# Performance work log

Measured on AMD Instinct MI355X. Metric: run time of the kernel, lower is better.

The kernel has to match this reference:

```python
import jax, jax.numpy as jnp
import numpy as np

B, T, H, W, D = 8, 16, 64, 64, 256
DK = 128
TOP_K = 4
DECAY = 0.95
TAU = 1.0
EPS = 1e-10


def setup_inputs() -> dict:
    key = jax.random.key(0)
    ks = jax.random.split(key, 6)
    return {
        "query_features": jax.random.normal(ks[0], (B, H, W, D), dtype=jnp.float32),
        "history_buffer": jax.random.normal(ks[1], (B, T, H, W, D), dtype=jnp.float32),
        "W_q": jax.random.normal(ks[2], (D, DK), dtype=jnp.float32) * (1.0 / np.sqrt(D)),
        "W_k": jax.random.normal(ks[3], (D, DK), dtype=jnp.float32) * (1.0 / np.sqrt(D)),
        "W_v": jax.random.normal(ks[4], (D, DK), dtype=jnp.float32) * (1.0 / np.sqrt(D)),
        "W_o": jax.random.normal(ks[5], (DK, D), dtype=jnp.float32) * (1.0 / np.sqrt(DK)),
    }


def reference(query_features, history_buffer, W_q, W_k, W_v, W_o):
    # Projections (Linear, bias=False)
    Q = jnp.einsum("bhwd,dk->bhwk", query_features, W_q)          # [B,H,W,DK]
    K = jnp.einsum("bthwd,dk->bthwk", history_buffer, W_k)        # [B,T,H,W,DK]
    V = jnp.einsum("bthwd,dk->bthwk", history_buffer, W_v)        # [B,T,H,W,DK]

    # Per-pixel temporal scores over T history steps
    scores = jnp.einsum("bhwk,bthwk->bhwt", Q, K) / jnp.sqrt(jnp.float32(DK))  # [B,H,W,T]

    # Top-K gating over the time axis (top_k < T)
    _, topk_idx = jax.lax.top_k(scores, TOP_K)                    # [B,H,W,K]
    mask = jax.nn.one_hot(topk_idx, T, dtype=scores.dtype).sum(axis=-2) > 0  # [B,H,W,T]
    scores = jnp.where(mask, scores, -jnp.inf)

    # Log-decay bias: decay_rate ** (T - t)
    t = jnp.arange(T, dtype=jnp.float32)
    decay_bias = jnp.log(jnp.float32(DECAY) ** (T - t) + EPS)     # [T]
    scores = scores + decay_bias

    attn = jax.nn.softmax(scores / TAU, axis=-1)                  # [B,H,W,T]

    out = jnp.einsum("bhwt,bthwk->bhwk", attn, V)                 # [B,H,W,DK]
    out = jnp.einsum("bhwk,kd->bhwd", out, W_o)                   # [B,H,W,D]
    return out
```

## Files before the change

kernel.cpp:

```cpp
#include <hip/hip_runtime.h>
#include <math.h>


typedef __attribute__((ext_vector_type(8))) short bf16x8;
typedef __attribute__((ext_vector_type(4))) float f32x4;

__device__ inline unsigned short f2bf(float f) {
  union { float f; unsigned u; } v; v.f = f;
  unsigned r = (v.u + 0x7FFF + ((v.u >> 16) & 1)) >> 16;
  return (unsigned short)r;
}

__global__ __launch_bounds__(256) void precompute_weights(
    const float* __restrict__ Wq, const float* __restrict__ Wk,
    const float* __restrict__ Wv, const float* __restrict__ Wo,
    float* __restrict__ M1, unsigned short* __restrict__ M2F) {
  __shared__ float rowbuf[128];
  int bid = blockIdx.x, tid = threadIdx.x;
  if (bid < 256) {
    if (tid < 128) rowbuf[tid] = Wq[bid * 128 + tid];
    __syncthreads();
    const float4* Wk4 = (const float4*)Wk;
    const float4* rb4 = (const float4*)rowbuf;
    float acc = 0.f;
#pragma unroll 8
    for (int k4 = 0; k4 < 32; ++k4) {
      float4 a = rb4[k4];
      float4 b = Wk4[tid * 32 + k4];
      acc = fmaf(a.x, b.x, acc); acc = fmaf(a.y, b.y, acc);
      acc = fmaf(a.z, b.z, acc); acc = fmaf(a.w, b.w, acc);
    }
    M1[bid * 256 + tid] = acc;
  } else {
    int k = bid - 256;
    if (tid < 128) rowbuf[tid] = Wv[k * 128 + tid];
    __syncthreads();
    float acc = 0.f;
#pragma unroll 8
    for (int kk = 0; kk < 128; ++kk)
      acc = fmaf(rowbuf[kk], Wo[kk * 256 + tid], acc);
    int c = tid;
    int ct = c >> 4, kt = k >> 5, lh = (k >> 3) & 3, i = k & 7, lm = c & 15;
    M2F[(size_t)(((ct * 8 + kt) * 64 + lh * 16 + lm) * 8 + i)] = f2bf(acc);
  }
}

__global__ __launch_bounds__(256, 2) void fused_all(
    const float* __restrict__ query, const float* __restrict__ hist,
    const float* __restrict__ M1, const unsigned short* __restrict__ M2F,
    float* __restrict__ OUT) {
  __shared__ float As[64][260];
  int tid = threadIdx.x;
  int l = tid & 63;
  int w = tid >> 6;
  int pix0 = blockIdx.x * 64;

  const float4* H4 = (const float4*)hist;
  int b = pix0 >> 12;
  int off0 = pix0 & 4095;
  size_t hblk = ((size_t)b * 16 * 4096 + off0) * 64 + l;
  int t_mine = l & 15;
  int gbase = l & 48;

  {
    const float4* Qb4 = (const float4*)(query + (size_t)pix0 * 256);
#pragma unroll
    for (int k = 0; k < 16; ++k)
      *(float4*)&As[w + 4 * k][4 * l] = Qb4[(size_t)(w + 4 * k) * 64 + l];
    float4 acc[16];
#pragma unroll
    for (int j = 0; j < 16; ++j) acc[j] = make_float4(0.f, 0.f, 0.f, 0.f);
    const float4* B4 = (const float4*)M1;
#pragma unroll 4
    for (int d = 0; d < 256; ++d) {
      float4 bv = B4[d * 64 + l];
#pragma unroll
      for (int j = 0; j < 16; ++j) {
        float a = As[w + 4 * j][d];
        acc[j].x = fmaf(a, bv.x, acc[j].x);
        acc[j].y = fmaf(a, bv.y, acc[j].y);
        acc[j].z = fmaf(a, bv.z, acc[j].z);
        acc[j].w = fmaf(a, bv.w, acc[j].w);
      }
    }
#pragma unroll
    for (int j = 0; j < 16; ++j)
      *(float4*)&As[w + 4 * j][4 * l] = acc[j];
  }

  float4 hA[16], hB[16];
#pragma unroll
  for (int t = 0; t < 16; ++t)
    hA[t] = H4[hblk + (size_t)w * 64 + (size_t)t * 262144];

#define ATTN_STEP(HC, HN, IT, DOPRE)                                        \
  {                                                                         \
    int row = w + 4 * (IT);                                                 \
    if (DOPRE) {                   \
      size_t nb = hblk + (size_t)(row + 4) * 64;                            \
      _Pragma("unroll") for (int t = 0; t < 16; ++t)                        \
          HN[t] = H4[nb + (size_t)t * 262144];                              \
    }                                                                       \
    float4 q = *(const float4*)&As[row][4 * l];                             \
    float part[16];                                                         \
    _Pragma("unroll") for (int t = 0; t < 16; ++t) {                        \
      float s = HC[t].x * q.x;                                              \
      s = fmaf(HC[t].y, q.y, s);                                            \
      s = fmaf(HC[t].z, q.z, s);                                            \
      s = fmaf(HC[t].w, q.w, s);                                            \
      part[t] = s;                                                          \
    }                                                                       \
    _Pragma("unroll") for (int st = 0; st < 4; ++st) {                      \
      bool hi = (l >> st) & 1;                                              \
      int nt = 8 >> st;                                                     \
      _Pragma("unroll") for (int i = 0; i < nt; ++i) {                      \
        float mine = hi ? part[2 * i + 1] : part[2 * i];                    \
        float oth = hi ? part[2 * i] : part[2 * i + 1];                     \
        part[i] = mine + __shfl_xor(oth, 1 << st);                          \
      }                                                                     \
    }                                                                       \
    float v = part[0];                                                      \
    v += __shfl_xor(v, 16);                                                 \
    v += __shfl_xor(v, 32);                                                 \
    float sc = v * 0.08838834764831845f;         \
    int rank = 0;              \
    _Pragma("unroll") for (int k = 1; k < 16; ++k) {                        \
      int ot = (t_mine + k) & 15;                                           \
      float o = __shfl(sc, gbase | ot);                                     \
      rank += (o > sc) || (o == sc && ot < t_mine);                         \
    }                                                                       \
    bool chosen = rank < 4;                                                 \
    float earg = sc + (float)(16 - t_mine) * -0.05129329438755058f;         \
    float ex = chosen ? expf(earg) : 0.0f;                                  \
    float Z = ex;                                                           \
    Z += __shfl_xor(Z, 1);                                                  \
    Z += __shfl_xor(Z, 2);                                                  \
    Z += __shfl_xor(Z, 4);                                                  \
    Z += __shfl_xor(Z, 8);                                                  \
    float attn = ex / Z;                                                    \
    float4 hb = make_float4(0.f, 0.f, 0.f, 0.f);                            \
    _Pragma("unroll") for (int t = 0; t < 16; ++t) {                        \
      float a = __shfl(attn, gbase | t);  \
      if (a != 0.0f) {                                                      \
        hb.x = fmaf(a, HC[t].x, hb.x);                                      \
        hb.y = fmaf(a, HC[t].y, hb.y);                                      \
        hb.z = fmaf(a, HC[t].z, hb.z);                                      \
        hb.w = fmaf(a, HC[t].w, hb.w);                                      \
      }                                                                     \
    }                                                                       \
    *(float4*)&As[row][4 * l] = hb;   \
  }

  for (int it2 = 0; it2 < 8; ++it2) {
    ATTN_STEP(hA, hB, 2 * it2, true);
    ATTN_STEP(hB, hA, 2 * it2 + 1, it2 < 7);
  }
#undef ATTN_STEP

  {
    int lm = l & 15, lh = l >> 4;
    const bf16x8* B8 = (const bf16x8*)M2F;
    f32x4 acc[16];
#pragma unroll
    for (int ct = 0; ct < 16; ++ct) acc[ct] = (f32x4){0.f, 0.f, 0.f, 0.f};
#pragma unroll
    for (int kt = 0; kt < 8; ++kt) {
      const float* ap = &As[w + 4 * lm][kt * 32 + lh * 8];
      float4 a0 = *(const float4*)ap;
      float4 a1 = *(const float4*)(ap + 4);
      bf16x8 afrag;
      afrag[0] = (short)f2bf(a0.x); afrag[1] = (short)f2bf(a0.y);
      afrag[2] = (short)f2bf(a0.z); afrag[3] = (short)f2bf(a0.w);
      afrag[4] = (short)f2bf(a1.x); afrag[5] = (short)f2bf(a1.y);
      afrag[6] = (short)f2bf(a1.z); afrag[7] = (short)f2bf(a1.w);
#pragma unroll
      for (int ct = 0; ct < 16; ++ct) {
        bf16x8 bfrag = B8[(ct * 8 + kt) * 64 + l];
        acc[ct] = __builtin_amdgcn_mfma_f32_16x16x32_bf16(afrag, bfrag,
                                                          acc[ct], 0, 0, 0);
      }
    }
    float* outp = OUT + (size_t)pix0 * 256;
#pragma unroll
    for (int ct = 0; ct < 16; ++ct) {
#pragma unroll
      for (int j = 0; j < 4; ++j)
        outp[(size_t)(w + 4 * (lh * 4 + j)) * 256 + ct * 16 + lm] =
            acc[ct][j];
    }
  }
}

extern "C" void kernel_launch(void* const* d_in, const int* in_sizes, int n_in,
                              void* d_out, int out_size, void* d_ws,
                              size_t ws_size, hipStream_t stream) {
  const float* query = (const float*)d_in[0];
  const float* hist = (const float*)d_in[1];
  const float* Wq = (const float*)d_in[2];
  const float* Wk = (const float*)d_in[3];
  const float* Wv = (const float*)d_in[4];
  const float* Wo = (const float*)d_in[5];
  float* out = (float*)d_out;

  float* ws = (float*)d_ws;
  float* M1 = ws;
  unsigned short* M2F = (unsigned short*)(ws + 65536);

  precompute_weights<<<512, 256, 0, stream>>>(Wq, Wk, Wv, Wo, M1, M2F);
  fused_all<<<512, 256, 0, stream>>>(query, hist, M1, M2F, out);
}
```

Baseline: 170.7 us.

## Stream history per time step with running top-4 selection per pixel

New measurement: 185.5 us. 8.7% more time.

```diff
diff --git a/kernel.cpp b/kernel.cpp
--- a/kernel.cpp
+++ b/kernel.cpp
@@ -54,19 +54,22 @@
   int l = tid & 63;
   int w = tid >> 6;
   int pix0 = blockIdx.x * 64;
+  int r0 = w * 16;
 
   const float4* H4 = (const float4*)hist;
   int b = pix0 >> 12;
   int off0 = pix0 & 4095;
-  size_t hblk = ((size_t)b * 16 * 4096 + off0) * 64 + l;
-  int t_mine = l & 15;
-  int gbase = l & 48;
+  size_t habase = ((size_t)b * 65536 + off0 + r0) * 64 + l;
+
+  float4 hA[4], hB[4];
+#pragma unroll
+  for (int j = 0; j < 4; ++j) hA[j] = H4[habase + (size_t)j * 64];
 
   {
     const float4* Qb4 = (const float4*)(query + (size_t)pix0 * 256);
 #pragma unroll
     for (int k = 0; k < 16; ++k)
-      *(float4*)&As[w + 4 * k][4 * l] = Qb4[(size_t)(w + 4 * k) * 64 + l];
+      *(float4*)&As[r0 + k][4 * l] = Qb4[(size_t)(r0 + k) * 64 + l];
     float4 acc[16];
 #pragma unroll
     for (int j = 0; j < 16; ++j) acc[j] = make_float4(0.f, 0.f, 0.f, 0.f);
@@ -76,7 +79,7 @@
       float4 bv = B4[d * 64 + l];
 #pragma unroll
       for (int j = 0; j < 16; ++j) {
-        float a = As[w + 4 * j][d];
+        float a = As[r0 + j][d];
         acc[j].x = fmaf(a, bv.x, acc[j].x);
         acc[j].y = fmaf(a, bv.y, acc[j].y);
         acc[j].z = fmaf(a, bv.z, acc[j].z);
@@ -85,77 +88,108 @@
     }
 #pragma unroll
     for (int j = 0; j < 16; ++j)
-      *(float4*)&As[w + 4 * j][4 * l] = acc[j];
-  }
-
-  float4 hA[16], hB[16];
-#pragma unroll
-  for (int t = 0; t < 16; ++t)
-    hA[t] = H4[hblk + (size_t)w * 64 + (size_t)t * 262144];
-
-#define ATTN_STEP(HC, HN, IT, DOPRE)                                        \
+      *(float4*)&As[r0 + j][4 * l] = acc[j];
+  }
+
+#define STEP(HC, HN, T, PRE, NG4, NT)                                       \
   {                                                                         \
-    int row = w + 4 * (IT);                                                 \
-    if (DOPRE) {                   \
-      size_t nb = hblk + (size_t)(row + 4) * 64;                            \
-      _Pragma("unroll") for (int t = 0; t < 16; ++t)                        \
-          HN[t] = H4[nb + (size_t)t * 262144];                              \
-    }                                                                       \
-    float4 q = *(const float4*)&As[row][4 * l];                             \
-    float part[16];                                                         \
-    _Pragma("unroll") for (int t = 0; t < 16; ++t) {                        \
-      float s = HC[t].x * q.x;                                              \
-      s = fmaf(HC[t].y, q.y, s);                                            \
-      s = fmaf(HC[t].z, q.z, s);                                            \
-      s = fmaf(HC[t].w, q.w, s);                                            \
-      part[t] = s;                                                          \
-    }                                                                       \
-    _Pragma("unroll") for (int st = 0; st < 4; ++st) {                      \
-      bool hi = (l >> st) & 1;                                              \
-      int nt = 8 >> st;                                                     \
-      _Pragma("unroll") for (int i = 0; i < nt; ++i) {                      \
-        float mine = hi ? part[2 * i + 1] : part[2 * i];                    \
-        float oth = hi ? part[2 * i] : part[2 * i + 1];                     \
-        part[i] = mine + __shfl_xor(oth, 1 << st);                          \
+    if (PRE) {                                                              \
+      _Pragma("unroll") for (int j = 0; j < 4; ++j)                         \
+          HN[j] = H4[habase + (size_t)((NG4) + j) * 64 +                    \
+                     (size_t)(NT)*262144];                                  \
+    }                                                                       \
+    float pp[4];                                                            \
+    _Pragma("unroll") for (int j = 0; j < 4; ++j) {                         \
+      float s = HC[j].x * q[j].x;                                           \
+      s = fmaf(HC[j].y, q[j].y, s);                                         \
+      s = fmaf(HC[j].z, q[j].z, s);                                         \
+      s = fmaf(HC[j].w, q[j].w, s);                                         \
+      pp[j] = s;                                                            \
+    }                                                                       \
+    float sc[4];                                                            \
+    {                                                                       \
+      bool h1 = l & 1;                                                      \
+      float m0 = h1 ? pp[1] : pp[0], o0 = h1 ? pp[0] : pp[1];               \
+      float r0v = m0 + __shfl_xor(o0, 1);                                   \
+      float m1 = h1 ? pp[3] : pp[2], o1 = h1 ? pp[2] : pp[3];               \
+      float r1v = m1 + __shfl_xor(o1, 1);                                   \
+      bool h2 = l & 2;                                                      \
+      float m2 = h2 ? r1v : r0v, o2 = h2 ? r0v : r1v;                       \
+      float rr = m2 + __shfl_xor(o2, 2);                                    \
+      rr += __shfl_xor(rr, 4);                                              \
+      rr += __shfl_xor(rr, 8);                                              \
+      rr += __shfl_xor(rr, 16);                                             \
+      rr += __shfl_xor(rr, 32);                                             \
+      rr *= 0.08838834764831845f;                          \
+      _Pragma("unroll") for (int j = 0; j < 4; ++j)                         \
+          sc[j] = __shfl(rr, (l & 60) | j);                                 \
+    }                                                                       \
+    _Pragma("unroll") for (int j = 0; j < 4; ++j) {                         \
+      if ((T) < 4) {                                        \
+        ss[j][(T)] = sc[j]; stf[j][(T)] = (float)(T); sh[j][(T)] = HC[j];   \
+      } else {       \
+        float ms = ss[j][0], mt = stf[j][0]; int m = 0;                     \
+        _Pragma("unroll") for (int k = 1; k < 4; ++k) {                     \
+          bool wse = (ss[j][k] < ms) || (ss[j][k] == ms && stf[j][k] > mt); \
+          if (wse) { m = k; ms = ss[j][k]; mt = stf[j][k]; }                \
+        }                                                                   \
+        if (sc[j] > ms) {                          \
+          _Pragma("unroll") for (int k = 0; k < 4; ++k)                     \
+              if (m == k) {                                                 \
+            ss[j][k] = sc[j]; stf[j][k] = (float)(T); sh[j][k] = HC[j];     \
+          }                                                                 \
+        }                                                                   \
       }                                                                     \
     }                                                                       \
-    float v = part[0];                                                      \
-    v += __shfl_xor(v, 16);                                                 \
-    v += __shfl_xor(v, 32);                                                 \
-    float sc = v * 0.08838834764831845f;         \
-    int rank = 0;              \
-    _Pragma("unroll") for (int k = 1; k < 16; ++k) {                        \
-      int ot = (t_mine + k) & 15;                                           \
-      float o = __shfl(sc, gbase | ot);                                     \
-      rank += (o > sc) || (o == sc && ot < t_mine);                         \
-    }                                                                       \
-    bool chosen = rank < 4;                                                 \
-    float earg = sc + (float)(16 - t_mine) * -0.05129329438755058f;         \
-    float ex = chosen ? expf(earg) : 0.0f;                                  \
-    float Z = ex;                                                           \
-    Z += __shfl_xor(Z, 1);                                                  \
-    Z += __shfl_xor(Z, 2);                                                  \
-    Z += __shfl_xor(Z, 4);                                                  \
-    Z += __shfl_xor(Z, 8);                                                  \
-    float attn = ex / Z;                                                    \
-    float4 hb = make_float4(0.f, 0.f, 0.f, 0.f);                            \
-    _Pragma("unroll") for (int t = 0; t < 16; ++t) {                        \
-      float a = __shfl(attn, gbase | t);  \
-      if (a != 0.0f) {                                                      \
-        hb.x = fmaf(a, HC[t].x, hb.x);                                      \
-        hb.y = fmaf(a, HC[t].y, hb.y);                                      \
-        hb.z = fmaf(a, HC[t].z, hb.z);                                      \
-        hb.w = fmaf(a, HC[t].w, hb.w);                                      \
-      }                                                                     \
-    }                                                                       \
-    *(float4*)&As[row][4 * l] = hb;   \
-  }
-
-  for (int it2 = 0; it2 < 8; ++it2) {
-    ATTN_STEP(hA, hB, 2 * it2, true);
-    ATTN_STEP(hB, hA, 2 * it2 + 1, it2 < 7);
-  }
-#undef ATTN_STEP
+  }
+
+  for (int g = 0; g < 4; ++g) {
+    int g4 = g * 4;
+    float4 q[4];
+#pragma unroll
+    for (int j = 0; j < 4; ++j)
+      q[j] = *(const float4*)&As[r0 + g4 + j][4 * l];
+    float ss[4][4], stf[4][4];
+    float4 sh[4][4];
+
+    STEP(hA, hB, 0, 1, g4, 1)
+    STEP(hB, hA, 1, 1, g4, 2)
+    STEP(hA, hB, 2, 1, g4, 3)
+    STEP(hB, hA, 3, 1, g4, 4)
+    STEP(hA, hB, 4, 1, g4, 5)
+    STEP(hB, hA, 5, 1, g4, 6)
+    STEP(hA, hB, 6, 1, g4, 7)
+    STEP(hB, hA, 7, 1, g4, 8)
+    STEP(hA, hB, 8, 1, g4, 9)
+    STEP(hB, hA, 9, 1, g4, 10)
+    STEP(hA, hB, 10, 1, g4, 11)
+    STEP(hB, hA, 11, 1, g4, 12)
+    STEP(hA, hB, 12, 1, g4, 13)
+    STEP(hB, hA, 13, 1, g4, 14)
+    STEP(hA, hB, 14, 1, g4, 15)
+    STEP(hB, hA, 15, (g < 3), g4 + 4, 0)
+
+#pragma unroll
+    for (int j = 0; j < 4; ++j) {
+      float e0 = expf(ss[j][0] + (16.f - stf[j][0]) * -0.05129329438755058f);
+      float e1 = expf(ss[j][1] + (16.f - stf[j][1]) * -0.05129329438755058f);
+      float e2 = expf(ss[j][2] + (16.f - stf[j][2]) * -0.05129329438755058f);
+      float e3 = expf(ss[j][3] + (16.f - stf[j][3]) * -0.05129329438755058f);
+      float iZ = 1.0f / (e0 + e1 + e2 + e3);
+      float a0 = e0 * iZ, a1 = e1 * iZ, a2 = e2 * iZ, a3 = e3 * iZ;
+      float4 hb;
+      hb.x = a0 * sh[j][0].x; hb.y = a0 * sh[j][0].y;
+      hb.z = a0 * sh[j][0].z; hb.w = a0 * sh[j][0].w;
+      hb.x = fmaf(a1, sh[j][1].x, hb.x); hb.y = fmaf(a1, sh[j][1].y, hb.y);
+      hb.z = fmaf(a1, sh[j][1].z, hb.z); hb.w = fmaf(a1, sh[j][1].w, hb.w);
+      hb.x = fmaf(a2, sh[j][2].x, hb.x); hb.y = fmaf(a2, sh[j][2].y, hb.y);
+      hb.z = fmaf(a2, sh[j][2].z, hb.z); hb.w = fmaf(a2, sh[j][2].w, hb.w);
+      hb.x = fmaf(a3, sh[j][3].x, hb.x); hb.y = fmaf(a3, sh[j][3].y, hb.y);
+      hb.z = fmaf(a3, sh[j][3].z, hb.z); hb.w = fmaf(a3, sh[j][3].w, hb.w);
+      *(float4*)&As[r0 + g4 + j][4 * l] = hb;
+    }
+  }
+#undef STEP
 
   {
     int lm = l & 15, lh = l >> 4;
@@ -165,7 +199,7 @@
     for (int ct = 0; ct < 16; ++ct) acc[ct] = (f32x4){0.f, 0.f, 0.f, 0.f};
 #pragma unroll
     for (int kt = 0; kt < 8; ++kt) {
-      const float* ap = &As[w + 4 * lm][kt * 32 + lh * 8];
+      const float* ap = &As[r0 + lm][kt * 32 + lh * 8];
       float4 a0 = *(const float4*)ap;
       float4 a1 = *(const float4*)(ap + 4);
       bf16x8 afrag;
@@ -185,8 +219,7 @@
     for (int ct = 0; ct < 16; ++ct) {
 #pragma unroll
       for (int j = 0; j < 4; ++j)
-        outp[(size_t)(w + 4 * (lh * 4 + j)) * 256 + ct * 16 + lm] =
-            acc[ct][j];
+        outp[(size_t)(r0 + lh * 4 + j) * 256 + ct * 16 + lm] = acc[ct][j];
     }
   }
 }
```

## Split attention into score pass and sparse top-k gather of history rows

Applied to the files above, without the earlier changes.

Result: slower. 197.8 us (+15.9%).

```diff
diff --git a/kernel.cpp b/kernel.cpp
--- a/kernel.cpp
+++ b/kernel.cpp
@@ -50,15 +50,19 @@
     const float* __restrict__ M1, const unsigned short* __restrict__ M2F,
     float* __restrict__ OUT) {
   __shared__ float As[64][260];
+  __shared__ float scoresS[64][17];
+  __shared__ float attnW[64][4];
+  __shared__ int attnT[64][4];
   int tid = threadIdx.x;
   int l = tid & 63;
   int w = tid >> 6;
   int pix0 = blockIdx.x * 64;
+  int r0 = w * 16;
 
   const float4* H4 = (const float4*)hist;
   int b = pix0 >> 12;
   int off0 = pix0 & 4095;
-  size_t hblk = ((size_t)b * 16 * 4096 + off0) * 64 + l;
+  int bT = b * 16;
   int t_mine = l & 15;
   int gbase = l & 48;
 
@@ -66,7 +70,7 @@
     const float4* Qb4 = (const float4*)(query + (size_t)pix0 * 256);
 #pragma unroll
     for (int k = 0; k < 16; ++k)
-      *(float4*)&As[w + 4 * k][4 * l] = Qb4[(size_t)(w + 4 * k) * 64 + l];
+      *(float4*)&As[r0 + k][4 * l] = Qb4[(size_t)(r0 + k) * 64 + l];
     float4 acc[16];
 #pragma unroll
     for (int j = 0; j < 16; ++j) acc[j] = make_float4(0.f, 0.f, 0.f, 0.f);
@@ -76,7 +80,7 @@
       float4 bv = B4[d * 64 + l];
 #pragma unroll
       for (int j = 0; j < 16; ++j) {
-        float a = As[w + 4 * j][d];
+        float a = As[r0 + j][d];
         acc[j].x = fmaf(a, bv.x, acc[j].x);
         acc[j].y = fmaf(a, bv.y, acc[j].y);
         acc[j].z = fmaf(a, bv.z, acc[j].z);
@@ -85,77 +89,108 @@
     }
 #pragma unroll
     for (int j = 0; j < 16; ++j)
-      *(float4*)&As[w + 4 * j][4 * l] = acc[j];
-  }
-
-  float4 hA[16], hB[16];
-#pragma unroll
-  for (int t = 0; t < 16; ++t)
-    hA[t] = H4[hblk + (size_t)w * 64 + (size_t)t * 262144];
-
-#define ATTN_STEP(HC, HN, IT, DOPRE)                                        \
-  {                                                                         \
-    int row = w + 4 * (IT);                                                 \
-    if (DOPRE) {                   \
-      size_t nb = hblk + (size_t)(row + 4) * 64;                            \
-      _Pragma("unroll") for (int t = 0; t < 16; ++t)                        \
-          HN[t] = H4[nb + (size_t)t * 262144];                              \
-    }                                                                       \
-    float4 q = *(const float4*)&As[row][4 * l];                             \
-    float part[16];                                                         \
-    _Pragma("unroll") for (int t = 0; t < 16; ++t) {                        \
-      float s = HC[t].x * q.x;                                              \
-      s = fmaf(HC[t].y, q.y, s);                                            \
-      s = fmaf(HC[t].z, q.z, s);                                            \
-      s = fmaf(HC[t].w, q.w, s);                                            \
-      part[t] = s;                                                          \
-    }                                                                       \
-    _Pragma("unroll") for (int st = 0; st < 4; ++st) {                      \
-      bool hi = (l >> st) & 1;                                              \
-      int nt = 8 >> st;                                                     \
-      _Pragma("unroll") for (int i = 0; i < nt; ++i) {                      \
-        float mine = hi ? part[2 * i + 1] : part[2 * i];                    \
-        float oth = hi ? part[2 * i] : part[2 * i + 1];                     \
-        part[i] = mine + __shfl_xor(oth, 1 << st);                          \
-      }                                                                     \
-    }                                                                       \
-    float v = part[0];                                                      \
-    v += __shfl_xor(v, 16);                                                 \
-    v += __shfl_xor(v, 32);                                                 \
-    float sc = v * 0.08838834764831845f;         \
-    int rank = 0;              \
-    _Pragma("unroll") for (int k = 1; k < 16; ++k) {                        \
-      int ot = (t_mine + k) & 15;                                           \
-      float o = __shfl(sc, gbase | ot);                                     \
-      rank += (o > sc) || (o == sc && ot < t_mine);                         \
-    }                                                                       \
-    bool chosen = rank < 4;                                                 \
-    float earg = sc + (float)(16 - t_mine) * -0.05129329438755058f;         \
-    float ex = chosen ? expf(earg) : 0.0f;                                  \
-    float Z = ex;                                                           \
-    Z += __shfl_xor(Z, 1);                                                  \
-    Z += __shfl_xor(Z, 2);                                                  \
-    Z += __shfl_xor(Z, 4);                                                  \
-    Z += __shfl_xor(Z, 8);                                                  \
-    float attn = ex / Z;                                                    \
-    float4 hb = make_float4(0.f, 0.f, 0.f, 0.f);                            \
-    _Pragma("unroll") for (int t = 0; t < 16; ++t) {                        \
-      float a = __shfl(attn, gbase | t);  \
-      if (a != 0.0f) {                                                      \
-        hb.x = fmaf(a, HC[t].x, hb.x);                                      \
-        hb.y = fmaf(a, HC[t].y, hb.y);                                      \
-        hb.z = fmaf(a, HC[t].z, hb.z);                                      \
-        hb.w = fmaf(a, HC[t].w, hb.w);                                      \
-      }                                                                     \
-    }                                                                       \
-    *(float4*)&As[row][4 * l] = hb;   \
-  }
-
-  for (int it2 = 0; it2 < 8; ++it2) {
-    ATTN_STEP(hA, hB, 2 * it2, true);
-    ATTN_STEP(hB, hA, 2 * it2 + 1, it2 < 7);
-  }
-#undef ATTN_STEP
+      *(float4*)&As[r0 + j][4 * l] = acc[j];
+  }
+  __syncthreads();
+
+  for (int tt = 0; tt < 4; ++tt) {
+    int t = w + 4 * tt;
+    size_t base = ((size_t)(bT + t) * 4096 + off0) * 64 + l;
+    float4 h[8], hn[8];
+#pragma unroll
+    for (int j = 0; j < 8; ++j) h[j] = H4[base + (size_t)j * 64];
+    for (int p8 = 0; p8 < 8; ++p8) {
+      if (p8 < 7) {
+#pragma unroll
+        for (int j = 0; j < 8; ++j)
+          hn[j] = H4[base + (size_t)(p8 * 8 + 8 + j) * 64];
+      }
+#pragma unroll
+      for (int j = 0; j < 8; ++j) {
+        int p = p8 * 8 + j;
+        float4 q = *(const float4*)&As[p][4 * l];
+        float s = h[j].x * q.x;
+        s = fmaf(h[j].y, q.y, s);
+        s = fmaf(h[j].z, q.z, s);
+        s = fmaf(h[j].w, q.w, s);
+        s += __shfl_xor(s, 1);
+        s += __shfl_xor(s, 2);
+        s += __shfl_xor(s, 4);
+        s += __shfl_xor(s, 8);
+        s += __shfl_xor(s, 16);
+        s += __shfl_xor(s, 32);
+        if (l == 0) scoresS[p][t] = s * 0.08838834764831845f;
+      }
+#pragma unroll
+      for (int j = 0; j < 8; ++j) h[j] = hn[j];
+    }
+  }
+  __syncthreads();
+
+#pragma unroll
+  for (int i = 0; i < 4; ++i) {
+    int p = r0 + 4 * i + (l >> 4);
+    float sc = scoresS[p][t_mine];
+    int rank = 0;
+#pragma unroll
+    for (int k = 1; k < 16; ++k) {
+      int ot = (t_mine + k) & 15;
+      float o = __shfl(sc, gbase | ot);
+      rank += (o > sc) || (o == sc && ot < t_mine);
+    }
+    bool chosen = rank < 4;
+    float earg = sc + (float)(16 - t_mine) * -0.05129329438755058f;
+    float ex = chosen ? expf(earg) : 0.0f;
+    float Z = ex;
+    Z += __shfl_xor(Z, 1);
+    Z += __shfl_xor(Z, 2);
+    Z += __shfl_xor(Z, 4);
+    Z += __shfl_xor(Z, 8);
+    unsigned long long bal = __ballot(chosen);
+    int before =
+        __popcll(bal & (((1ull << l) - 1)) & (0xFFFFull << gbase));
+    if (chosen) {
+      attnW[p][before] = ex / Z;
+      attnT[p][before] = t_mine;
+    }
+  }
+
+#pragma unroll 2
+  for (int i = 0; i < 16; i += 2) {
+    int p0 = r0 + i;
+    float aW[2][4];
+    int aT[2][4];
+#pragma unroll
+    for (int u = 0; u < 2; ++u)
+#pragma unroll
+      for (int j = 0; j < 4; ++j) {
+        aW[u][j] = attnW[p0 + u][j];
+        aT[u][j] = attnT[p0 + u][j];
+      }
+    float4 hv[2][4];
+#pragma unroll
+    for (int u = 0; u < 2; ++u)
+#pragma unroll
+      for (int j = 0; j < 4; ++j)
+        hv[u][j] =
+            H4[((size_t)(bT + aT[u][j]) * 4096 + off0 + p0 + u) * 64 + l];
+#pragma unroll
+    for (int u = 0; u < 2; ++u) {
+      float4 acc;
+      acc.x = aW[u][0] * hv[u][0].x;
+      acc.y = aW[u][0] * hv[u][0].y;
+      acc.z = aW[u][0] * hv[u][0].z;
+      acc.w = aW[u][0] * hv[u][0].w;
+#pragma unroll
+      for (int j = 1; j < 4; ++j) {
+        acc.x = fmaf(aW[u][j], hv[u][j].x, acc.x);
+        acc.y = fmaf(aW[u][j], hv[u][j].y, acc.y);
+        acc.z = fmaf(aW[u][j], hv[u][j].z, acc.z);
+        acc.w = fmaf(aW[u][j], hv[u][j].w, acc.w);
+      }
+      *(float4*)&As[p0 + u][4 * l] = acc;
+    }
+  }
 
   {
     int lm = l & 15, lh = l >> 4;
@@ -165,7 +200,7 @@
     for (int ct = 0; ct < 16; ++ct) acc[ct] = (f32x4){0.f, 0.f, 0.f, 0.f};
 #pragma unroll
     for (int kt = 0; kt < 8; ++kt) {
-      const float* ap = &As[w + 4 * lm][kt * 32 + lh * 8];
+      const float* ap = &As[r0 + lm][kt * 32 + lh * 8];
       float4 a0 = *(const float4*)ap;
       float4 a1 = *(const float4*)(ap + 4);
       bf16x8 afrag;
@@ -185,8 +220,7 @@
     for (int ct = 0; ct < 16; ++ct) {
 #pragma unroll
       for (int j = 0; j < 4; ++j)
-        outp[(size_t)(w + 4 * (lh * 4 + j)) * 256 + ct * 16 + lm] =
-            acc[ct][j];
+        outp[(size_t)(r0 + lh * 4 + j) * 256 + ct * 16 + lm] = acc[ct][j];
     }
   }
 }
```

## Compute query projection with split-bf16 MFMA emulation of fp32 GEMM

Applied to the files above, without the earlier changes.

New measurement: 158.5 us. 7.2% less time.

```diff
diff --git a/kernel.cpp b/kernel.cpp
--- a/kernel.cpp
+++ b/kernel.cpp
@@ -10,15 +10,21 @@
   unsigned r = (v.u + 0x7FFF + ((v.u >> 16) & 1)) >> 16;
   return (unsigned short)r;
 }
+__device__ inline float bf2f(unsigned short h) {
+  union { unsigned u; float f; } v; v.u = ((unsigned)h) << 16;
+  return v.f;
+}
 
 __global__ __launch_bounds__(256) void precompute_weights(
     const float* __restrict__ Wq, const float* __restrict__ Wk,
     const float* __restrict__ Wv, const float* __restrict__ Wo,
-    float* __restrict__ M1, unsigned short* __restrict__ M2F) {
+    unsigned short* __restrict__ M1A, unsigned short* __restrict__ M1B,
+    unsigned short* __restrict__ M1C, unsigned short* __restrict__ M2F) {
   __shared__ float rowbuf[128];
   int bid = blockIdx.x, tid = threadIdx.x;
   if (bid < 256) {
-    if (tid < 128) rowbuf[tid] = Wq[bid * 128 + tid];
+    int d = bid;
+    if (tid < 128) rowbuf[tid] = Wq[d * 128 + tid];
     __syncthreads();
     const float4* Wk4 = (const float4*)Wk;
     const float4* rb4 = (const float4*)rowbuf;
@@ -30,7 +36,16 @@
       acc = fmaf(a.x, b.x, acc); acc = fmaf(a.y, b.y, acc);
       acc = fmaf(a.z, b.z, acc); acc = fmaf(a.w, b.w, acc);
     }
-    M1[bid * 256 + tid] = acc;
+    int c = tid;
+    int ct = c >> 4, kt = d >> 5, lh = (d >> 3) & 3, i = d & 7, lm = c & 15;
+    size_t idx = (size_t)(((ct * 8 + kt) * 64 + lh * 16 + lm) * 8 + i);
+    unsigned short h0 = f2bf(acc);
+    float r1 = acc - bf2f(h0);
+    unsigned short h1 = f2bf(r1);
+    float r2 = r1 - bf2f(h1);
+    M1A[idx] = h0;
+    M1B[idx] = h1;
+    M1C[idx] = f2bf(r2);
   } else {
     int k = bid - 256;
     if (tid < 128) rowbuf[tid] = Wv[k * 128 + tid];
@@ -47,13 +62,16 @@
 
 __global__ __launch_bounds__(256, 2) void fused_all(
     const float* __restrict__ query, const float* __restrict__ hist,
-    const float* __restrict__ M1, const unsigned short* __restrict__ M2F,
-    float* __restrict__ OUT) {
+    const unsigned short* __restrict__ M1A,
+    const unsigned short* __restrict__ M1B,
+    const unsigned short* __restrict__ M1C,
+    const unsigned short* __restrict__ M2F, float* __restrict__ OUT) {
   __shared__ float As[64][260];
   int tid = threadIdx.x;
   int l = tid & 63;
   int w = tid >> 6;
   int pix0 = blockIdx.x * 64;
+  int lm = l & 15, lh = l >> 4;
 
   const float4* H4 = (const float4*)hist;
   int b = pix0 >> 12;
@@ -62,36 +80,75 @@
   int t_mine = l & 15;
   int gbase = l & 48;
 
-  {
-    const float4* Qb4 = (const float4*)(query + (size_t)pix0 * 256);
-#pragma unroll
-    for (int k = 0; k < 16; ++k)
-      *(float4*)&As[w + 4 * k][4 * l] = Qb4[(size_t)(w + 4 * k) * 64 + l];
-    float4 acc[16];
-#pragma unroll
-    for (int j = 0; j < 16; ++j) acc[j] = make_float4(0.f, 0.f, 0.f, 0.f);
-    const float4* B4 = (const float4*)M1;
-#pragma unroll 4
-    for (int d = 0; d < 256; ++d) {
-      float4 bv = B4[d * 64 + l];
-#pragma unroll
-      for (int j = 0; j < 16; ++j) {
-        float a = As[w + 4 * j][d];
-        acc[j].x = fmaf(a, bv.x, acc[j].x);
-        acc[j].y = fmaf(a, bv.y, acc[j].y);
-        acc[j].z = fmaf(a, bv.z, acc[j].z);
-        acc[j].w = fmaf(a, bv.w, acc[j].w);
-      }
-    }
-#pragma unroll
-    for (int j = 0; j < 16; ++j)
-      *(float4*)&As[w + 4 * j][4 * l] = acc[j];
-  }
-
   float4 hA[16], hB[16];
 #pragma unroll
   for (int t = 0; t < 16; ++t)
     hA[t] = H4[hblk + (size_t)w * 64 + (size_t)t * 262144];
+
+  {
+    const float* Qb = query + (size_t)pix0 * 256;
+    for (int i = tid; i < 64 * 256; i += 256)
+      As[i >> 8][i & 255] = Qb[i];
+    __syncthreads();
+
+    const bf16x8* BA = (const bf16x8*)M1A;
+    const bf16x8* BB = (const bf16x8*)M1B;
+    const bf16x8* BC = (const bf16x8*)M1C;
+    f32x4 qacc[16];
+#pragma unroll
+    for (int i = 0; i < 16; ++i) qacc[i] = (f32x4){0.f, 0.f, 0.f, 0.f};
+#pragma unroll
+    for (int kt = 0; kt < 8; ++kt) {
+      bf16x8 qa[4], qb[4], qc[4];
+#pragma unroll
+      for (int rt = 0; rt < 4; ++rt) {
+        const float* ap = &As[rt * 16 + lm][kt * 32 + lh * 8];
+        float4 a0 = *(const float4*)ap;
+        float4 a1 = *(const float4*)(ap + 4);
+        float av[8] = {a0.x, a0.y, a0.z, a0.w, a1.x, a1.y, a1.z, a1.w};
+#pragma unroll
+        for (int e = 0; e < 8; ++e) {
+          unsigned short h0 = f2bf(av[e]);
+          float r1 = av[e] - bf2f(h0);
+          unsigned short h1 = f2bf(r1);
+          float r2 = r1 - bf2f(h1);
+          qa[rt][e] = (short)h0;
+          qb[rt][e] = (short)h1;
+          qc[rt][e] = (short)f2bf(r2);
+        }
+      }
+#pragma unroll
+      for (int cc = 0; cc < 4; ++cc) {
+        int ct = w * 4 + cc;
+        bf16x8 ba = BA[(ct * 8 + kt) * 64 + l];
+        bf16x8 bb = BB[(ct * 8 + kt) * 64 + l];
+        bf16x8 bc = BC[(ct * 8 + kt) * 64 + l];
+#pragma unroll
+        for (int rt = 0; rt < 4; ++rt) {
+          f32x4 a = qacc[rt * 4 + cc];
+          a = __builtin_amdgcn_mfma_f32_16x16x32_bf16(qa[rt], ba, a, 0, 0, 0);
+          a = __builtin_amdgcn_mfma_f32_16x16x32_bf16(qa[rt], bb, a, 0, 0, 0);
+          a = __builtin_amdgcn_mfma_f32_16x16x32_bf16(qb[rt], ba, a, 0, 0, 0);
+          a = __builtin_amdgcn_mfma_f32_16x16x32_bf16(qa[rt], bc, a, 0, 0, 0);
+          a = __builtin_amdgcn_mfma_f32_16x16x32_bf16(qb[rt], bb, a, 0, 0, 0);
+          a = __builtin_amdgcn_mfma_f32_16x16x32_bf16(qc[rt], ba, a, 0, 0, 0);
+          a = __builtin_amdgcn_mfma_f32_16x16x32_bf16(qb[rt], bc, a, 0, 0, 0);
+          a = __builtin_amdgcn_mfma_f32_16x16x32_bf16(qc[rt], bb, a, 0, 0, 0);
+          qacc[rt * 4 + cc] = a;
+        }
+      }
+    }
+    __syncthreads();
+#pragma unroll
+    for (int rt = 0; rt < 4; ++rt)
+#pragma unroll
+      for (int cc = 0; cc < 4; ++cc)
+#pragma unroll
+        for (int j = 0; j < 4; ++j)
+          As[rt * 16 + lh * 4 + j][w * 64 + cc * 16 + lm] =
+              qacc[rt * 4 + cc][j];
+    __syncthreads();
+  }
 
 #define ATTN_STEP(HC, HN, IT, DOPRE)                                        \
   {                                                                         \
@@ -158,7 +215,6 @@
 #undef ATTN_STEP
 
   {
-    int lm = l & 15, lh = l >> 4;
     const bf16x8* B8 = (const bf16x8*)M2F;
     f32x4 acc[16];
 #pragma unroll
@@ -202,10 +258,13 @@
   const float* Wo = (const float*)d_in[5];
   float* out = (float*)d_out;
 
-  float* ws = (float*)d_ws;
-  float* M1 = ws;
-  unsigned short* M2F = (unsigned short*)(ws + 65536);
-
-  precompute_weights<<<512, 256, 0, stream>>>(Wq, Wk, Wv, Wo, M1, M2F);
-  fused_all<<<512, 256, 0, stream>>>(query, hist, M1, M2F, out);
-}
+  unsigned short* wsu = (unsigned short*)d_ws;
+  unsigned short* M1A = wsu;
+  unsigned short* M1B = wsu + 65536;
+  unsigned short* M1C = wsu + 131072;
+  unsigned short* M2F = wsu + 196608;
+
+  precompute_weights<<<512, 256, 0, stream>>>(Wq, Wk, Wv, Wo, M1A, M1B, M1C,
+                                              M2F);
+  fused_all<<<512, 256, 0, stream>>>(query, hist, M1A, M1B, M1C, M2F, out);
+}
```
